# Optimization experiments

Measured on AMD Instinct MI355X. Metric: run time of the kernel, lower is better.

## Reference

```python
import jax, jax.numpy as jnp
import numpy as np

D_MODEL = 4096
NUM_EXPERTS = 64
TOP_K = 2


def setup_inputs() -> dict:
    key = jax.random.key(0)
    kx, kw, kb = jax.random.split(key, 3)
    x = jax.random.normal(kx, (4, 4096, D_MODEL), dtype=jnp.float32)
    # nn.Linear default init ~ U(-1/sqrt(fan_in), 1/sqrt(fan_in))
    bound = 1.0 / np.sqrt(D_MODEL)
    W = jax.random.uniform(kw, (D_MODEL, NUM_EXPERTS), minval=-bound, maxval=bound, dtype=jnp.float32)
    b = jax.random.uniform(kb, (NUM_EXPERTS,), minval=-bound, maxval=bound, dtype=jnp.float32)
    return {"x": x, "W": W, "b": b}


def reference(x, W, b):
    # gate: [B,S,D] @ [D,E] -> [B,S,E]
    logits = jnp.einsum('bsd,de->bse', x, W) + b
    probs = jax.nn.softmax(logits, axis=-1)
    topk_probs, topk_indices = jax.lax.top_k(probs, TOP_K)
    topk_probs = topk_probs / (jnp.sum(topk_probs, axis=-1, keepdims=True) + 1e-9)
    return probs, topk_probs, topk_indices
```

## Files before the change

kernel.cpp:

```cpp
#include <hip/hip_runtime.h>

#define D_MODEL 4096
#define NEXP    64
#define NTOK    16384
#define NKS     128

typedef _Float16 half8 __attribute__((ext_vector_type(8)));
typedef float    f32x4 __attribute__((ext_vector_type(4)));

__device__ __forceinline__ void split8(float4 a, float4 b, half8& hi, half8& lo) {
    auto h0 = __builtin_amdgcn_cvt_pkrtz(a.x, a.y);
    auto h1 = __builtin_amdgcn_cvt_pkrtz(a.z, a.w);
    auto h2 = __builtin_amdgcn_cvt_pkrtz(b.x, b.y);
    auto h3 = __builtin_amdgcn_cvt_pkrtz(b.z, b.w);
    hi[0] = static_cast<_Float16>(h0[0]); hi[1] = static_cast<_Float16>(h0[1]);
    hi[2] = static_cast<_Float16>(h1[0]); hi[3] = static_cast<_Float16>(h1[1]);
    hi[4] = static_cast<_Float16>(h2[0]); hi[5] = static_cast<_Float16>(h2[1]);
    hi[6] = static_cast<_Float16>(h3[0]); hi[7] = static_cast<_Float16>(h3[1]);
    float r0 = a.x - (float)h0[0], r1 = a.y - (float)h0[1];
    float r2 = a.z - (float)h1[0], r3 = a.w - (float)h1[1];
    float r4 = b.x - (float)h2[0], r5 = b.y - (float)h2[1];
    float r6 = b.z - (float)h3[0], r7 = b.w - (float)h3[1];
    auto l0 = __builtin_amdgcn_cvt_pkrtz(r0, r1);
    auto l1 = __builtin_amdgcn_cvt_pkrtz(r2, r3);
    auto l2 = __builtin_amdgcn_cvt_pkrtz(r4, r5);
    auto l3 = __builtin_amdgcn_cvt_pkrtz(r6, r7);
    lo[0] = static_cast<_Float16>(l0[0]); lo[1] = static_cast<_Float16>(l0[1]);
    lo[2] = static_cast<_Float16>(l1[0]); lo[3] = static_cast<_Float16>(l1[1]);
    lo[4] = static_cast<_Float16>(l2[0]); lo[5] = static_cast<_Float16>(l2[1]);
    lo[6] = static_cast<_Float16>(l3[0]); lo[7] = static_cast<_Float16>(l3[1]);
}

__global__ __launch_bounds__(256) void prep_w(const float* __restrict__ W,
                                              half8* __restrict__ ws) {
    const int gid  = blockIdx.x * 256 + threadIdx.x;
    const int lane = gid & 63;
    const int fp   = gid >> 6;
    const int t    = fp & 3;
    const int ks   = fp >> 2;
    const int e    = 16 * t + (lane & 15);
    const int k0   = ks * 32 + (lane >> 4) * 8;
    float4 a, b;
    a.x = W[(size_t)(k0 + 0) * NEXP + e];
    a.y = W[(size_t)(k0 + 1) * NEXP + e];
    a.z = W[(size_t)(k0 + 2) * NEXP + e];
    a.w = W[(size_t)(k0 + 3) * NEXP + e];
    b.x = W[(size_t)(k0 + 4) * NEXP + e];
    b.y = W[(size_t)(k0 + 5) * NEXP + e];
    b.z = W[(size_t)(k0 + 6) * NEXP + e];
    b.w = W[(size_t)(k0 + 7) * NEXP + e];
    half8 hi, lo;
    split8(a, b, hi, lo);
    ws[(size_t)(fp * 2 + 0) * 64 + lane] = hi;
    ws[(size_t)(fp * 2 + 1) * 64 + lane] = lo;
}

__global__ __launch_bounds__(256, 1) void router_mfma(
    const float* __restrict__ x, const int4* __restrict__ wf,
    const float* __restrict__ b, float* __restrict__ out)
{
    __shared__ float ls[4][16][68];
    const int tid  = threadIdx.x;
    const int lane = tid & 63;
    const int wv   = tid >> 6;
    const int tok0 = blockIdx.x * 64 + wv * 16;
    const int m    = lane & 15;
    const int q    = lane >> 4;
    const float* __restrict__ xrow = x + (size_t)(tok0 + m) * D_MODEL + q * 8;

    f32x4 acc[4] = {};

    float4 xc[2][2], xn[2][2];
    int4   wc[2][4][2], wn[2][4][2];

    auto ldx = [&](int c, float4 dst[2][2]) {
#pragma unroll
        for (int s = 0; s < 2; s++) {
            const float* p = xrow + (c * 2 + s) * 32;
            dst[s][0] = *(const float4*)p;
            dst[s][1] = *(const float4*)(p + 4);
        }
    };
    auto ldw = [&](int c, int4 dst[2][4][2]) {
#pragma unroll
        for (int s = 0; s < 2; s++) {
            const int ks = c * 2 + s;
#pragma unroll
            for (int t = 0; t < 4; t++) {
                const int fi = (ks * 4 + t) * 2;
                dst[s][t][0] = wf[(size_t)fi * 64 + lane];
                dst[s][t][1] = wf[(size_t)(fi + 1) * 64 + lane];
            }
        }
    };

    ldx(0, xc);
    ldw(0, wc);
#pragma unroll 1
    for (int c = 0; c < 64; c++) {
        const int nc = (c < 63) ? c + 1 : 0;
        ldx(nc, xn);
        ldw(nc, wn);
#pragma unroll
        for (int s = 0; s < 2; s++) {
            half8 ahi, alo;
            split8(xc[s][0], xc[s][1], ahi, alo);
#pragma unroll
            for (int t = 0; t < 4; t++) {
                half8 bhi = __builtin_bit_cast(half8, wc[s][t][0]);
                half8 blo = __builtin_bit_cast(half8, wc[s][t][1]);
                acc[t] = __builtin_amdgcn_mfma_f32_16x16x32_f16(ahi, bhi, acc[t], 0, 0, 0);
                acc[t] = __builtin_amdgcn_mfma_f32_16x16x32_f16(ahi, blo, acc[t], 0, 0, 0);
                acc[t] = __builtin_amdgcn_mfma_f32_16x16x32_f16(alo, bhi, acc[t], 0, 0, 0);
            }
        }
#pragma unroll
        for (int s = 0; s < 2; s++) {
            xc[s][0] = xn[s][0]; xc[s][1] = xn[s][1];
#pragma unroll
            for (int t = 0; t < 4; t++) {
                wc[s][t][0] = wn[s][t][0];
                wc[s][t][1] = wn[s][t][1];
            }
        }
    }

#pragma unroll
    for (int t = 0; t < 4; t++)
#pragma unroll
        for (int r = 0; r < 4; r++)
            ls[wv][q * 4 + r][t * 16 + m] = acc[t][r];

    const float bias = b[lane];
    float* __restrict__ probs_out = out;
    float* __restrict__ top_out   = out + (size_t)NTOK * NEXP;
    float* __restrict__ idx_out   = top_out + (size_t)NTOK * 2;

#pragma unroll 1
    for (int r2 = 0; r2 < 16; r2++) {
        const int token = tok0 + r2;
        float logit = ls[wv][r2][lane] + bias;

        float mx = logit;
#pragma unroll
        for (int off = 32; off; off >>= 1) mx = fmaxf(mx, __shfl_xor(mx, off, 64));
        float ex = expf(logit - mx);
        float s = ex;
#pragma unroll
        for (int off = 32; off; off >>= 1) s += __shfl_xor(s, off, 64);
        float p = ex / s;
        probs_out[(size_t)token * NEXP + lane] = p;

        float v = p; int idx = lane;
#pragma unroll
        for (int off = 32; off; off >>= 1) {
            float ov = __shfl_xor(v, off, 64);
            int   oi = __shfl_xor(idx, off, 64);
            if (ov > v || (ov == v && oi < idx)) { v = ov; idx = oi; }
        }
        const float v1 = v; const int i1 = idx;
        v = (lane == i1) ? -1.0f : p; idx = lane;
#pragma unroll
        for (int off = 32; off; off >>= 1) {
            float ov = __shfl_xor(v, off, 64);
            int   oi = __shfl_xor(idx, off, 64);
            if (ov > v || (ov == v && oi < idx)) { v = ov; idx = oi; }
        }
        const float v2 = v; const int i2 = idx;

        if (lane == 0) {
            const float dnm = v1 + v2 + 1e-9f;
            top_out[(size_t)token * 2 + 0] = v1 / dnm;
            top_out[(size_t)token * 2 + 1] = v2 / dnm;
            idx_out[(size_t)token * 2 + 0] = (float)i1;
            idx_out[(size_t)token * 2 + 1] = (float)i2;
        }
    }
}

#define BK  128
#define BKP (BK + 4)
__device__ __forceinline__ float rl(float v, int l) {
    return __int_as_float(__builtin_amdgcn_readlane(__float_as_int(v), l));
}
__global__ __launch_bounds__(128) void router_fallback(
    const float* __restrict__ x, const float* __restrict__ W,
    const float* __restrict__ b, float* __restrict__ out)
{
    __shared__ float wt[NEXP * BKP];
    const int tid  = threadIdx.x;
    const int lane = tid & 63;
    const int wv   = __builtin_amdgcn_readfirstlane(tid >> 6);
    const int tok0 = blockIdx.x * 16 + wv * 8;
    const float* __restrict__ xw = x + (size_t)tok0 * D_MODEL;

    float2 xcur[8], xnxt[8];
#pragma unroll
    for (int t = 0; t < 8; t++)
        xcur[t] = *(const float2*)(xw + (size_t)t * D_MODEL + 2 * lane);
    float accm[8];
#pragma unroll
    for (int t = 0; t < 8; t++) accm[t] = 0.f;

    for (int c = 0; c < D_MODEL / BK; c++) {
        const int k0 = c * BK;
        if (c + 1 < D_MODEL / BK) {
#pragma unroll
            for (int t = 0; t < 8; t++)
                xnxt[t] = *(const float2*)(xw + (size_t)t * D_MODEL + (k0 + BK) + 2 * lane);
        }
#pragma unroll
        for (int i = 0; i < 16; i++) {
            int n  = i * 128 + tid;
            int dd = n >> 4;
            int e0 = (n & 15) * 4;
            float4 v = *(const float4*)(W + (size_t)(k0 + dd) * NEXP + e0);
            wt[(e0 + 0) * BKP + dd] = v.x;
            wt[(e0 + 1) * BKP + dd] = v.y;
            wt[(e0 + 2) * BKP + dd] = v.z;
            wt[(e0 + 3) * BKP + dd] = v.w;
        }
        __syncthreads();
        float acc[8];
#pragma unroll
        for (int t = 0; t < 8; t++) acc[t] = 0.f;
        const float* wl = &wt[lane * BKP];
#pragma unroll 4
        for (int kk = 0; kk < BK; kk += 4) {
            float4 w4 = *(const float4*)(wl + kk);
            const int l0 = kk >> 1;
#pragma unroll
            for (int t = 0; t < 8; t++) {
                float a = acc[t];
                a = fmaf(rl(xcur[t].x, l0    ), w4.x, a);
                a = fmaf(rl(xcur[t].y, l0    ), w4.y, a);
                a = fmaf(rl(xcur[t].x, l0 + 1), w4.z, a);
                a = fmaf(rl(xcur[t].y, l0 + 1), w4.w, a);
                acc[t] = a;
            }
        }
#pragma unroll
        for (int t = 0; t < 8; t++) accm[t] += acc[t];
        __syncthreads();
#pragma unroll
        for (int t = 0; t < 8; t++) xcur[t] = xnxt[t];
    }

    const float bias = b[lane];
    float* __restrict__ probs_out = out;
    float* __restrict__ top_out   = out + (size_t)NTOK * NEXP;
    float* __restrict__ idx_out   = top_out + (size_t)NTOK * 2;
#pragma unroll 1
    for (int t = 0; t < 8; t++) {
        const int token = tok0 + t;
        float logit = accm[t] + bias;
        float mx = logit;
#pragma unroll
        for (int off = 32; off; off >>= 1) mx = fmaxf(mx, __shfl_xor(mx, off, 64));
        float ex = expf(logit - mx);
        float s = ex;
#pragma unroll
        for (int off = 32; off; off >>= 1) s += __shfl_xor(s, off, 64);
        float p = ex / s;
        probs_out[(size_t)token * NEXP + lane] = p;
        float v = p; int idx = lane;
#pragma unroll
        for (int off = 32; off; off >>= 1) {
            float ov = __shfl_xor(v, off, 64);
            int   oi = __shfl_xor(idx, off, 64);
            if (ov > v || (ov == v && oi < idx)) { v = ov; idx = oi; }
        }
        const float v1 = v; const int i1 = idx;
        v = (lane == i1) ? -1.0f : p; idx = lane;
#pragma unroll
        for (int off = 32; off; off >>= 1) {
            float ov = __shfl_xor(v, off, 64);
            int   oi = __shfl_xor(idx, off, 64);
            if (ov > v || (ov == v && oi < idx)) { v = ov; idx = oi; }
        }
        const float v2 = v; const int i2 = idx;
        if (lane == 0) {
            const float dnm = v1 + v2 + 1e-9f;
            top_out[(size_t)token * 2 + 0] = v1 / dnm;
            top_out[(size_t)token * 2 + 1] = v2 / dnm;
            idx_out[(size_t)token * 2 + 0] = (float)i1;
            idx_out[(size_t)token * 2 + 1] = (float)i2;
        }
    }
}

extern "C" void kernel_launch(void* const* d_in, const int* in_sizes, int n_in,
                              void* d_out, int out_size, void* d_ws, size_t ws_size,
                              hipStream_t stream) {
    const float* x = (const float*)d_in[0];
    const float* W = (const float*)d_in[1];
    const float* b = (const float*)d_in[2];
    float* out = (float*)d_out;

    const size_t need = (size_t)NKS * 4 * 2 * 64 * 16;
    if (ws_size >= need) {
        prep_w<<<128, 256, 0, stream>>>(W, (half8*)d_ws);
        router_mfma<<<256, 256, 0, stream>>>(x, (const int4*)d_ws, b, out);
    } else {
        router_fallback<<<NTOK / 16, 128, 0, stream>>>(x, W, b, out);
    }
}
```

Measured before the change: 423.5 us.

## Split K dimension across waves and launch more blocks for occupancy

Each block now handles 16 tokens instead of 64, and its four waves each take a quarter of the 4096-wide reduction. The partial results are summed through shared memory after a barrier. The grid grows from 256 blocks to 1024, and launch bounds allow four blocks per CU, which should give more waves to hide memory latency. The cost is a shared-memory reduction plus a sync, and each block re-reads the full weight tile for only 16 tokens, so W traffic from L2 rises.

After: 414.3 us. -2.2%, faster.

```diff
diff --git a/kernel.cpp b/kernel.cpp
--- a/kernel.cpp
+++ b/kernel.cpp
@@ -55,81 +55,64 @@
     ws[(size_t)(fp * 2 + 1) * 64 + lane] = lo;
 }
 
-__global__ __launch_bounds__(256, 1) void router_mfma(
+__global__ __launch_bounds__(256, 4) void router_mfma(
     const float* __restrict__ x, const int4* __restrict__ wf,
     const float* __restrict__ b, float* __restrict__ out)
 {
-    __shared__ float ls[4][16][68];
+    __shared__ float part[4][16][68];
     const int tid  = threadIdx.x;
     const int lane = tid & 63;
     const int wv   = tid >> 6;
-    const int tok0 = blockIdx.x * 64 + wv * 16;
+    const int tok0 = blockIdx.x * 16;
     const int m    = lane & 15;
     const int q    = lane >> 4;
-    const float* __restrict__ xrow = x + (size_t)(tok0 + m) * D_MODEL + q * 8;
+    const float* __restrict__ xrow =
+        x + (size_t)(tok0 + m) * D_MODEL + wv * 1024 + q * 8;
 
     f32x4 acc[4] = {};
 
-    float4 xc[2][2], xn[2][2];
-    int4   wc[2][4][2], wn[2][4][2];
-
-    auto ldx = [&](int c, float4 dst[2][2]) {
-#pragma unroll
-        for (int s = 0; s < 2; s++) {
-            const float* p = xrow + (c * 2 + s) * 32;
-            dst[s][0] = *(const float4*)p;
-            dst[s][1] = *(const float4*)(p + 4);
+    float4 xaA, xbA, xaB, xbB;
+    int4   wA[4][2], wB[4][2];
+
+    auto ldj = [&](int j, float4& xa, float4& xb, int4 (&w)[4][2]) {
+        const float* p = xrow + j * 32;
+        xa = *(const float4*)p;
+        xb = *(const float4*)(p + 4);
+        const size_t base = (size_t)(wv * 32 + j) * 512 + lane;
+#pragma unroll
+        for (int t = 0; t < 4; t++) {
+            w[t][0] = wf[base + t * 128];
+            w[t][1] = wf[base + t * 128 + 64];
         }
     };
-    auto ldw = [&](int c, int4 dst[2][4][2]) {
-#pragma unroll
-        for (int s = 0; s < 2; s++) {
-            const int ks = c * 2 + s;
-#pragma unroll
-            for (int t = 0; t < 4; t++) {
-                const int fi = (ks * 4 + t) * 2;
-                dst[s][t][0] = wf[(size_t)fi * 64 + lane];
-                dst[s][t][1] = wf[(size_t)(fi + 1) * 64 + lane];
-            }
+    auto cmp = [&](const float4& xa, const float4& xb, int4 (&w)[4][2]) {
+        half8 ahi, alo;
+        split8(xa, xb, ahi, alo);
+#pragma unroll
+        for (int t = 0; t < 4; t++) {
+            half8 bhi = __builtin_bit_cast(half8, w[t][0]);
+            half8 blo = __builtin_bit_cast(half8, w[t][1]);
+            acc[t] = __builtin_amdgcn_mfma_f32_16x16x32_f16(ahi, bhi, acc[t], 0, 0, 0);
+            acc[t] = __builtin_amdgcn_mfma_f32_16x16x32_f16(ahi, blo, acc[t], 0, 0, 0);
+            acc[t] = __builtin_amdgcn_mfma_f32_16x16x32_f16(alo, bhi, acc[t], 0, 0, 0);
         }
     };
 
-    ldx(0, xc);
-    ldw(0, wc);
+    ldj(0, xaA, xbA, wA);
 #pragma unroll 1
-    for (int c = 0; c < 64; c++) {
-        const int nc = (c < 63) ? c + 1 : 0;
-        ldx(nc, xn);
-        ldw(nc, wn);
-#pragma unroll
-        for (int s = 0; s < 2; s++) {
-            half8 ahi, alo;
-            split8(xc[s][0], xc[s][1], ahi, alo);
-#pragma unroll
-            for (int t = 0; t < 4; t++) {
-                half8 bhi = __builtin_bit_cast(half8, wc[s][t][0]);
-                half8 blo = __builtin_bit_cast(half8, wc[s][t][1]);
-                acc[t] = __builtin_amdgcn_mfma_f32_16x16x32_f16(ahi, bhi, acc[t], 0, 0, 0);
-                acc[t] = __builtin_amdgcn_mfma_f32_16x16x32_f16(ahi, blo, acc[t], 0, 0, 0);
-                acc[t] = __builtin_amdgcn_mfma_f32_16x16x32_f16(alo, bhi, acc[t], 0, 0, 0);
-            }
-        }
-#pragma unroll
-        for (int s = 0; s < 2; s++) {
-            xc[s][0] = xn[s][0]; xc[s][1] = xn[s][1];
-#pragma unroll
-            for (int t = 0; t < 4; t++) {
-                wc[s][t][0] = wn[s][t][0];
-                wc[s][t][1] = wn[s][t][1];
-            }
-        }
+    for (int j = 0; j < 32; j += 2) {
+        ldj(j + 1, xaB, xbB, wB);
+        cmp(xaA, xbA, wA);
+        ldj((j + 2) & 31, xaA, xbA, wA);
+        cmp(xaB, xbB, wB);
     }
 
 #pragma unroll
     for (int t = 0; t < 4; t++)
 #pragma unroll
         for (int r = 0; r < 4; r++)
-            ls[wv][q * 4 + r][t * 16 + m] = acc[t][r];
+            part[wv][q * 4 + r][t * 16 + m] = acc[t][r];
+    __syncthreads();
 
     const float bias = b[lane];
     float* __restrict__ probs_out = out;
@@ -137,9 +120,11 @@
     float* __restrict__ idx_out   = top_out + (size_t)NTOK * 2;
 
 #pragma unroll 1
-    for (int r2 = 0; r2 < 16; r2++) {
-        const int token = tok0 + r2;
-        float logit = ls[wv][r2][lane] + bias;
+    for (int r2 = 0; r2 < 4; r2++) {
+        const int row   = wv * 4 + r2;
+        const int token = tok0 + row;
+        float logit = part[0][row][lane] + part[1][row][lane]
+                    + part[2][row][lane] + part[3][row][lane] + bias;
 
         float mx = logit;
 #pragma unroll
@@ -300,7 +285,7 @@
     const size_t need = (size_t)NKS * 4 * 2 * 64 * 16;
     if (ws_size >= need) {
         prep_w<<<128, 256, 0, stream>>>(W, (half8*)d_ws);
-        router_mfma<<<256, 256, 0, stream>>>(x, (const int4*)d_ws, b, out);
+        router_mfma<<<NTOK / 16, 256, 0, stream>>>(x, (const int4*)d_ws, b, out);
     } else {
         router_fallback<<<NTOK / 16, 128, 0, stream>>>(x, W, b, out);
     }
```
